# Kernel optimization log

Measured on AMD Instinct MI355X. Metric: run time of the kernel, lower is better.

Reference implementation:

```python
import jax, jax.numpy as jnp
import numpy as np

SEQ_LEN = 128   # sourceL == seq_len
BATCH   = 256
E_DIM   = 512
H_DIM   = 512
C_EXPL  = 10.0  # tanh_exploration


def setup_inputs() -> dict:
    key = jax.random.key(0)
    ks = jax.random.split(key, 24)
    rn = lambda k, shape, s=0.05: (jax.random.normal(k, shape, jnp.float32) * s)
    inp = {
        'decoder_input':  rn(ks[0], (BATCH, E_DIM), 1.0),
        'embedded_inputs': rn(ks[1], (SEQ_LEN, BATCH, E_DIM), 1.0),
        'h0': rn(ks[2], (BATCH, H_DIM), 1.0),
        'c0': rn(ks[3], (BATCH, H_DIM), 1.0),
        'context': rn(ks[4], (SEQ_LEN, BATCH, H_DIM), 1.0),
        # LSTM cell weights (nn.Linear: y = x @ W.T + b)
        'Wi': rn(ks[5], (4 * H_DIM, E_DIM)), 'bi': rn(ks[6], (4 * H_DIM,)),
        'Wh': rn(ks[7], (4 * H_DIM, H_DIM)), 'bh': rn(ks[8], (4 * H_DIM,)),
        # glimpse attention (use_tanh=False)
        'g_Wq': rn(ks[9], (H_DIM, H_DIM)),  'g_bq': rn(ks[10], (H_DIM,)),
        'g_Wref': rn(ks[11], (H_DIM, H_DIM)), 'g_bref': rn(ks[12], (H_DIM,)),
        'g_v': rn(ks[13], (H_DIM,), 1.0 / np.sqrt(H_DIM)),
        # pointer attention (use_tanh=True, C=10)
        'p_Wq': rn(ks[14], (H_DIM, H_DIM)),  'p_bq': rn(ks[15], (H_DIM,)),
        'p_Wref': rn(ks[16], (H_DIM, H_DIM)), 'p_bref': rn(ks[17], (H_DIM,)),
        'p_v': rn(ks[18], (H_DIM,), 1.0 / np.sqrt(H_DIM)),
    }
    return inp


def reference(decoder_input, embedded_inputs, h0, c0, context,
              Wi, bi, Wh, bh,
              g_Wq, g_bq, g_Wref, g_bref, g_v,
              p_Wq, p_bq, p_Wref, p_bref, p_v):
    L, B, H = context.shape

    # Conv1d(k=1) on ref is loop-invariant: precompute e = W_ref @ context, [B,H,L]
    e_g = jnp.einsum('oh,lbh->bol', g_Wref, context) + g_bref[None, :, None]
    e_p = jnp.einsum('oh,lbh->bol', p_Wref, context) + p_bref[None, :, None]
    barange = jnp.arange(B)

    def step(carry, key):
        hx, cx, dec_in, mask, prev = carry
        # fused LSTM cell
        gates = dec_in @ Wi.T + bi + hx @ Wh.T + bh
        i_, f_, g_, o_ = jnp.split(gates, 4, axis=1)
        cy = jax.nn.sigmoid(f_) * cx + jax.nn.sigmoid(i_) * jnp.tanh(g_)
        hy = jax.nn.sigmoid(o_) * jnp.tanh(cy)
        # mark previously selected index as visited
        mask = mask.at[barange, prev].set(True)
        # glimpse (n_glimpses=1, use_tanh=False)
        q = hy @ g_Wq.T + g_bq                                   # [B,H]
        u = jnp.einsum('h,bhl->bl', g_v, jnp.tanh(q[:, :, None] + e_g))
        u = jnp.where(mask, -jnp.inf, u)
        g_l = jnp.einsum('bhl,bl->bh', e_g, jax.nn.softmax(u, axis=1))
        # pointer (use_tanh=True): logits = C * tanh(u), then mask
        q = g_l @ p_Wq.T + p_bq
        u = jnp.einsum('h,bhl->bl', p_v, jnp.tanh(q[:, :, None] + e_p))
        u = jnp.where(mask, -jnp.inf, C_EXPL * jnp.tanh(u))
        probs = jax.nn.softmax(u, axis=1)                        # [B,L]
        # stochastic decode: multinomial sample, gather next embedding
        idxs = jax.random.categorical(key, u, axis=1)            # [B]
        dec_next = embedded_inputs[idxs, barange, :]             # [B,E]
        return (hy, cy, dec_next, mask, idxs), (probs, idxs)

    mask0 = jnp.zeros((B, L), dtype=bool).at[:, 0].set(True)
    prev0 = jnp.zeros((B,), dtype=jnp.int32)
    keys = jax.random.split(jax.random.key(1), L - 1)
    (hy, cy, _, _, _), (probs_seq, idxs_seq) = jax.lax.scan(
        step, (h0, c0, decoder_input, mask0, prev0), keys)

    prob_0 = jnp.zeros((B, L), jnp.float32).at[:, 0].set(1.0)
    outputs = jnp.concatenate([prob_0[None], probs_seq], axis=0)          # [L,B,L]
    selections = jnp.concatenate([prev0[None], idxs_seq], axis=0)         # [L,B]
    return outputs, selections, hy, cy
```

## Files before the change

kernel.cpp:

```cpp
#include <hip/hip_runtime.h>
#include <stdint.h>

#ifndef THREEFRY_PARTITIONABLE
#define THREEFRY_PARTITIONABLE 1
#endif

#define LSEQ 128
#define BSZ  256
#define HD   512
#define G4   2048

#define SEL_OFF  ((size_t)LSEQ * BSZ * LSEQ)
#define HY_OFF   (SEL_OFF + (size_t)LSEQ * BSZ)
#define CY_OFF   (HY_OFF + (size_t)BSZ * HD)

__device__ __forceinline__ uint32_t rotl_(uint32_t v, int r) { return (v << r) | (v >> (32 - r)); }

__device__ __forceinline__ void tf2x32(uint32_t k0, uint32_t k1,
                                       uint32_t x0, uint32_t x1,
                                       uint32_t &o0, uint32_t &o1)
{
  uint32_t k2 = k0 ^ k1 ^ 0x1BD11BDAu;
  x0 += k0; x1 += k1;
#define TFR(r) { x0 += x1; x1 = rotl_(x1,(r)); x1 ^= x0; }
  TFR(13) TFR(15) TFR(26) TFR(6)
  x0 += k1; x1 += k2 + 1u;
  TFR(17) TFR(29) TFR(16) TFR(24)
  x0 += k2; x1 += k0 + 2u;
  TFR(13) TFR(15) TFR(26) TFR(6)
  x0 += k0; x1 += k1 + 3u;
  TFR(17) TFR(29) TFR(16) TFR(24)
  x0 += k1; x1 += k2 + 4u;
  TFR(13) TFR(15) TFR(26) TFR(6)
  x0 += k2; x1 += k0 + 5u;
#undef TFR
  o0 = x0; o1 = x1;
}

__device__ __forceinline__ void step_key(int t, uint32_t &kA, uint32_t &kB)
{
#if THREEFRY_PARTITIONABLE
  uint32_t o0, o1;
  tf2x32(0u, 1u, 0u, (uint32_t)t, o0, o1);
  kA = o0; kB = o1;
#else
  uint32_t o0, o1;
  uint32_t j = 2u * (uint32_t)t;
  if (j < 127u) { tf2x32(0u, 1u, j, 127u + j, o0, o1); kA = o0; }
  else          { tf2x32(0u, 1u, j - 127u, j, o0, o1); kA = o1; }
  j = 2u * (uint32_t)t + 1u;
  if (j < 127u) { tf2x32(0u, 1u, j, 127u + j, o0, o1); kB = o0; }
  else          { tf2x32(0u, 1u, j - 127u, j, o0, o1); kB = o1; }
#endif
}

__device__ __forceinline__ uint32_t draw_bits(uint32_t kA, uint32_t kB, uint32_t n)
{
  uint32_t y0, y1;
#if THREEFRY_PARTITIONABLE
  tf2x32(kA, kB, 0u, n, y0, y1);
  return y0 ^ y1;
#else
  uint32_t i0 = (n < 16384u) ? n : n - 16384u;
  tf2x32(kA, kB, i0, i0 + 16384u, y0, y1);
  return (n < 16384u) ? y0 : y1;
#endif
}

__device__ __forceinline__ float tanh_f(float xf)
{
  float ax = fabsf(xf);
  float z  = fminf(ax * 2.8853900817779268f, 50.0f);
  float e  = __builtin_amdgcn_exp2f(z);
  float d  = e + 1.0f;
  float r0 = __builtin_amdgcn_rcpf(d);
  float r  = fmaf(fmaf(-d, r0, 1.0f), r0, r0);
  return copysignf(fmaf(-2.0f, r, 1.0f), xf);
}

template<int CHUNK>
__global__ __launch_bounds__(512)
void gemm32(const float* __restrict__ A0, const float* __restrict__ A1, int lda,
            const float* __restrict__ B0, const float* __restrict__ B1, int ldb,
            const float* __restrict__ bias,
            double* __restrict__ Cd0, double* __restrict__ Cd1,
            float* __restrict__ Cf0, float* __restrict__ Cf1,
            int N, int K, int out_mode)
{
  constexpr int BM = 64;
  constexpr int BN = 64;
  constexpr int BK = 32;
  __shared__ float As[BK][BM];
  __shared__ float Bs[BK][BN];
  const int tid = threadIdx.x;
  const int tx = tid & 31, ty = tid >> 5;
  const int z = blockIdx.z;
  const float* A = z ? A1 : A0;
  const float* B = z ? B1 : B0;
  const int m0 = blockIdx.x * BM;
  const int n0 = blockIdx.y * BN;

  const int r_ = tid >> 3, kq = (tid & 7) * 4;

  double acc[4][2];
  float  c32[4][2];
#pragma unroll
  for (int i = 0; i < 4; ++i)
#pragma unroll
    for (int j = 0; j < 2; ++j) { acc[i][j] = 0.0; c32[i][j] = 0.0f; }

  const float* bp0 = B + (size_t)(n0 + r_) * ldb + kq;
  float4 w0 = *(const float4*)bp0;
  const float* ap0 = A + (size_t)(m0 + r_) * lda + kq;
  float4 u0 = *(const float4*)ap0;

  for (int k0 = 0; k0 < K; k0 += BK) {
    __syncthreads();
    Bs[kq + 0][r_] = w0.x; Bs[kq + 1][r_] = w0.y;
    Bs[kq + 2][r_] = w0.z; Bs[kq + 3][r_] = w0.w;
    As[kq + 0][r_] = u0.x; As[kq + 1][r_] = u0.y;
    As[kq + 2][r_] = u0.z; As[kq + 3][r_] = u0.w;
    __syncthreads();

    float4 nw0 = w0, nu0 = u0;
    if (k0 + BK < K) {
      nw0 = *(const float4*)(B + (size_t)(n0 + r_) * ldb + (k0 + BK) + kq);
      nu0 = *(const float4*)(A + (size_t)(m0 + r_) * lda + (k0 + BK) + kq);
    }

#pragma unroll
    for (int kk = 0; kk < BK; ++kk) {
      float4 av = *(const float4*)&As[kk][4 * ty];
      float2 bv = *(const float2*)&Bs[kk][2 * tx];
      float a[4] = { av.x, av.y, av.z, av.w };
#pragma unroll
      for (int i = 0; i < 4; ++i) {
        c32[i][0] = fmaf(a[i], bv.x, c32[i][0]);
        c32[i][1] = fmaf(a[i], bv.y, c32[i][1]);
      }
      if ((kk & (CHUNK - 1)) == (CHUNK - 1)) {
#pragma unroll
        for (int i = 0; i < 4; ++i)
#pragma unroll
          for (int j = 0; j < 2; ++j) { acc[i][j] += (double)c32[i][j]; c32[i][j] = 0.0f; }
      }
    }
    w0 = nw0; u0 = nu0;
  }

#pragma unroll
  for (int i = 0; i < 4; ++i) {
    int m = m0 + 4 * ty + i;
#pragma unroll
    for (int j = 0; j < 2; ++j) {
      int n = n0 + 2 * tx + j;
      double v = acc[i][j] + (bias ? (double)bias[n] : 0.0);
      if (out_mode == 0) {
        double* Cd = z ? Cd1 : Cd0;
        Cd[(size_t)m * N + n] = v;
      } else if (out_mode == 1) {
        Cf0[(((size_t)(m & 255)) * LSEQ + (m >> 8)) * HD + n] = (float)v;
      } else if (out_mode == 2) {
        Cf0[(size_t)m * N + n] = (float)v;
      } else if (out_mode == 3) {
        Cf0[(((size_t)(m & 255)) * HD + n) * LSEQ + (m >> 8)] = (float)v;
      } else {
        float* Cf = z ? Cf1 : Cf0;
        Cf[(size_t)m * N + n] = (float)v;
      }
    }
  }
}

__global__ __launch_bounds__(256)
void transpose512(const float* __restrict__ W, float* __restrict__ WT)
{
  __shared__ float tile[32][33];
  int bx = blockIdx.x * 32, by = blockIdx.y * 32;
  int x = threadIdx.x & 31, y = threadIdx.x >> 5;
#pragma unroll
  for (int j = 0; j < 32; j += 8)
    tile[y + j][x] = W[(size_t)(by + y + j) * HD + bx + x];
  __syncthreads();
#pragma unroll
  for (int j = 0; j < 32; j += 8)
    WT[(size_t)(bx + y + j) * HD + by + x] = tile[x][y + j];
}

#define SCOMP(A0_, A1_, A2_, A3_, V4, IT)                         \
  {                                                               \
    const int h_ = (IT) * 16 + hh;                                \
    const float  xq_ = (float)qs[h_];                             \
    const double vv_ = (double)vs[h_];                            \
    A0_ += vv_ * (double)tanh_f(xq_ + (V4).x);                    \
    A1_ += vv_ * (double)tanh_f(xq_ + (V4).y);                    \
    A2_ += vv_ * (double)tanh_f(xq_ + (V4).z);                    \
    A3_ += vv_ * (double)tanh_f(xq_ + (V4).w);                    \
  }

__global__ __launch_bounds__(512)
void step_fused(const float* __restrict__ g0, const float* __restrict__ g1,
                const float* __restrict__ bi, const float* __restrict__ bh,
                const double* __restrict__ c_in, double* __restrict__ c_out,
                float* __restrict__ h_out,
                const float* __restrict__ WqT, const float* __restrict__ g_bq,
                const float* __restrict__ e_g,
                const float* __restrict__ pWqT, const float* __restrict__ p_bq,
                const float* __restrict__ e_p,
                const float* __restrict__ g_v, const float* __restrict__ p_v,
                unsigned char* __restrict__ mask,
                const float* __restrict__ emb, float* __restrict__ dec_in,
                float* __restrict__ out, int t)
{
  const int b   = blockIdx.x;
  const int tid = threadIdx.x;
  const int l   = tid & 127;
  const int lg  = tid & 31;
  const int hh  = tid >> 5;
  __shared__ float  hs[HD];
  __shared__ double qs[HD];
  __shared__ float  vs[HD];
  __shared__ double part[16][LSEQ];
  __shared__ double gls[HD];
  __shared__ double sarr[LSEQ];
  __shared__ double red[4];
  __shared__ double wv[2];
  __shared__ int    wi[2];
  __shared__ int    selidx;

  const float* egbase = e_g + (size_t)b * (HD * LSEQ) + hh * LSEQ + lg * 4;
  const float* epbase = e_p + (size_t)b * (HD * LSEQ) + hh * LSEQ + lg * 4;

  float4 B0[8], B1[8];
#pragma unroll
  for (int j = 0; j < 8; ++j)
    B0[j] = *(const float4*)(egbase + (size_t)j * (16 * LSEQ));

  {
    const int u = tid;
    const size_t base = (size_t)b * G4;
    double gi = (double)g0[base + u]        + (double)g1[base + u]        + (double)bi[u]        + (double)bh[u];
    double gf = (double)g0[base + u + 512]  + (double)g1[base + u + 512]  + (double)bi[u + 512]  + (double)bh[u + 512];
    double gg = (double)g0[base + u + 1024] + (double)g1[base + u + 1024] + (double)bi[u + 1024] + (double)bh[u + 1024];
    double go = (double)g0[base + u + 1536] + (double)g1[base + u + 1536] + (double)bi[u + 1536] + (double)bh[u + 1536];
    double si = 1.0 / (1.0 + exp(-gi));
    double sf = 1.0 / (1.0 + exp(-gf));
    double so = 1.0 / (1.0 + exp(-go));
    double cy = sf * c_in[(size_t)b * HD + u] + si * tanh(gg);
    double hy = so * tanh(cy);
    c_out[(size_t)b * HD + u] = cy;
    float hyf = (float)hy;
    h_out[(size_t)b * HD + u] = hyf;
    hs[u] = hyf;
  }
  __syncthreads();

  {
    const int h = tid;
    const float* wcol = WqT + h;
    float wA[32], wB[32];
    double a = 0.0;
#pragma unroll
    for (int j = 0; j < 32; ++j) wA[j] = wcol[(size_t)j * HD];
#pragma unroll
    for (int pair = 0; pair < 8; ++pair) {
      const int kA = pair * 64;
#pragma unroll
      for (int j = 0; j < 32; ++j) wB[j] = wcol[(size_t)(kA + 32 + j) * HD];
#pragma unroll
      for (int c = 0; c < 4; ++c) {
        float c32 = 0.0f;
#pragma unroll
        for (int j = 0; j < 8; ++j)
          c32 = fmaf(hs[kA + c * 8 + j], wA[c * 8 + j], c32);
        a += (double)c32;
      }
      if (pair < 7) {
#pragma unroll
        for (int j = 0; j < 32; ++j) wA[j] = wcol[(size_t)(kA + 64 + j) * HD];
      }
#pragma unroll
      for (int c = 0; c < 4; ++c) {
        float c32 = 0.0f;
#pragma unroll
        for (int j = 0; j < 8; ++j)
          c32 = fmaf(hs[kA + 32 + c * 8 + j], wB[c * 8 + j], c32);
        a += (double)c32;
      }
    }
    qs[tid] = a + (double)g_bq[tid];
    vs[tid] = g_v[tid];
  }
  __syncthreads();

  {
    double a0 = 0, a1 = 0, a2 = 0, a3 = 0;
#pragma unroll
    for (int j = 0; j < 8; ++j)
      B1[j] = *(const float4*)(egbase + (size_t)(8 + j) * (16 * LSEQ));
#pragma unroll
    for (int j = 0; j < 8; ++j) SCOMP(a0, a1, a2, a3, B0[j], j);
#pragma unroll
    for (int j = 0; j < 8; ++j)
      B0[j] = *(const float4*)(egbase + (size_t)(16 + j) * (16 * LSEQ));
#pragma unroll
    for (int j = 0; j < 8; ++j) SCOMP(a0, a1, a2, a3, B1[j], 8 + j);
#pragma unroll
    for (int j = 0; j < 8; ++j)
      B1[j] = *(const float4*)(egbase + (size_t)(24 + j) * (16 * LSEQ));
#pragma unroll
    for (int j = 0; j < 8; ++j) SCOMP(a0, a1, a2, a3, B0[j], 16 + j);
#pragma unroll
    for (int j = 0; j < 8; ++j) SCOMP(a0, a1, a2, a3, B1[j], 24 + j);
    part[hh][lg * 4 + 0] = a0;
    part[hh][lg * 4 + 1] = a1;
    part[hh][lg * 4 + 2] = a2;
    part[hh][lg * 4 + 3] = a3;
  }
  __syncthreads();

  bool   msk = false;
  double u = 0.0, pe = 0.0;
  if (tid < 128) {
    msk = mask[(size_t)b * LSEQ + l] != 0;
    u = 0.0;
#pragma unroll
    for (int o = 0; o < 16; ++o) u += part[o][l];
    if (msk) u = -__builtin_inf();
    double mx = u;
    for (int off = 32; off; off >>= 1) mx = fmax(mx, __shfl_xor(mx, off));
    if ((tid & 63) == 0) red[tid >> 6] = mx;
  }
  __syncthreads();
  if (tid < 128) {
    double mx = fmax(red[0], red[1]);
    pe = msk ? 0.0 : exp(u - mx);
    double sm = pe;
    for (int off = 32; off; off >>= 1) sm += __shfl_xor(sm, off);
    if ((tid & 63) == 0) red[2 + (tid >> 6)] = sm;
  }
  __syncthreads();
  if (tid < 128) sarr[l] = pe / (red[2] + red[3]);
  __syncthreads();

  {
#pragma unroll
    for (int j = 0; j < 8; ++j)
      B0[j] = *(const float4*)(epbase + (size_t)j * (16 * LSEQ));

    const float4* row = (const float4*)(e_g + ((size_t)b * HD + tid) * LSEQ);
    float4 rA[4], rB[4];
    double a = 0.0;
#pragma unroll
    for (int j = 0; j < 4; ++j) rA[j] = row[j];
#pragma unroll
    for (int r = 0; r < 4; ++r) {
#pragma unroll
      for (int j = 0; j < 4; ++j) rB[j] = row[r * 8 + 4 + j];
#pragma unroll
      for (int j = 0; j < 4; ++j) {
        int l4 = (r * 8 + j) * 4;
        float4 v = rA[j];
        a += (double)v.x * sarr[l4 + 0];
        a += (double)v.y * sarr[l4 + 1];
        a += (double)v.z * sarr[l4 + 2];
        a += (double)v.w * sarr[l4 + 3];
      }
      if (r < 3) {
#pragma unroll
        for (int j = 0; j < 4; ++j) rA[j] = row[r * 8 + 8 + j];
      }
#pragma unroll
      for (int j = 0; j < 4; ++j) {
        int l4 = (r * 8 + 4 + j) * 4;
        float4 v = rB[j];
        a += (double)v.x * sarr[l4 + 0];
        a += (double)v.y * sarr[l4 + 1];
        a += (double)v.z * sarr[l4 + 2];
        a += (double)v.w * sarr[l4 + 3];
      }
    }
    gls[tid] = a;
  }
  __syncthreads();

  {
    const float* wcol = pWqT + tid;
    float wA[32], wB[32];
    double a = 0.0;
#pragma unroll
    for (int j = 0; j < 32; ++j) wA[j] = wcol[(size_t)j * HD];
#pragma unroll
    for (int pair = 0; pair < 8; ++pair) {
      const int hA = pair * 64;
#pragma unroll
      for (int j = 0; j < 32; ++j) wB[j] = wcol[(size_t)(hA + 32 + j) * HD];
#pragma unroll
      for (int j = 0; j < 32; ++j) a += gls[hA + j] * (double)wA[j];
      if (pair < 7) {
#pragma unroll
        for (int j = 0; j < 32; ++j) wA[j] = wcol[(size_t)(hA + 64 + j) * HD];
      }
#pragma unroll
      for (int j = 0; j < 32; ++j) a += gls[hA + 32 + j] * (double)wB[j];
    }
    qs[tid] = a + (double)p_bq[tid];
    vs[tid] = p_v[tid];
  }
  __syncthreads();

  {
    double a0 = 0, a1 = 0, a2 = 0, a3 = 0;
#pragma unroll
    for (int j = 0; j < 8; ++j)
      B1[j] = *(const float4*)(epbase + (size_t)(8 + j) * (16 * LSEQ));
#pragma unroll
    for (int j = 0; j < 8; ++j) SCOMP(a0, a1, a2, a3, B0[j], j);
#pragma unroll
    for (int j = 0; j < 8; ++j)
      B0[j] = *(const float4*)(epbase + (size_t)(16 + j) * (16 * LSEQ));
#pragma unroll
    for (int j = 0; j < 8; ++j) SCOMP(a0, a1, a2, a3, B1[j], 8 + j);
#pragma unroll
    for (int j = 0; j < 8; ++j)
      B1[j] = *(const float4*)(epbase + (size_t)(24 + j) * (16 * LSEQ));
#pragma unroll
    for (int j = 0; j < 8; ++j) SCOMP(a0, a1, a2, a3, B0[j], 16 + j);
#pragma unroll
    for (int j = 0; j < 8; ++j) SCOMP(a0, a1, a2, a3, B1[j], 24 + j);
    part[hh][lg * 4 + 0] = a0;
    part[hh][lg * 4 + 1] = a1;
    part[hh][lg * 4 + 2] = a2;
    part[hh][lg * 4 + 3] = a3;
  }
  __syncthreads();

  double logit = 0.0, cand = 0.0;
  int idx = l;
  if (tid < 128) {
    double acc2 = 0.0;
#pragma unroll
    for (int o = 0; o < 16; ++o) acc2 += part[o][l];
    logit = msk ? -__builtin_inf() : 10.0 * tanh(acc2);
    double mx = logit;
    for (int off = 32; off; off >>= 1) mx = fmax(mx, __shfl_xor(mx, off));
    if ((tid & 63) == 0) red[tid >> 6] = mx;
  }
  __syncthreads();
  if (tid < 128) {
    double mx = fmax(red[0], red[1]);
    double pe2 = msk ? 0.0 : exp(logit - mx);
    double sm = pe2;
    for (int off = 32; off; off >>= 1) sm += __shfl_xor(sm, off);
    if ((tid & 63) == 0) red[2 + (tid >> 6)] = sm;
  }
  __syncthreads();
  if (tid < 128) {
    double mx = fmax(red[0], red[1]);
    double pe2 = msk ? 0.0 : exp(logit - mx);
    out[(size_t)(t + 1) * BSZ * LSEQ + (size_t)b * LSEQ + l] = (float)(pe2 / (red[2] + red[3]));

    uint32_t kA, kB;
    step_key(t, kA, kB);
    uint32_t bits = draw_bits(kA, kB, (uint32_t)(b * LSEQ + l));
    float f = __uint_as_float((bits >> 9) | 0x3f800000u) - 1.0f;
    const float TINY = 1.17549435e-38f;
    float uu = fmaxf(f * (1.0f - TINY) + TINY, TINY);
    float gmb = -logf(-logf(uu));
    cand = msk ? -__builtin_inf() : (logit + (double)gmb);

    for (int off = 32; off; off >>= 1) {
      double c2 = __shfl_xor(cand, off);
      int    i2 = __shfl_xor(idx, off);
      if (c2 > cand || (c2 == cand && i2 < idx)) { cand = c2; idx = i2; }
    }
    if ((tid & 63) == 0) { wv[tid >> 6] = cand; wi[tid >> 6] = idx; }
  }
  __syncthreads();
  if (tid == 0) {
    double c2 = wv[1]; int i2 = wi[1];
    if (c2 > cand || (c2 == cand && i2 < idx)) { cand = c2; idx = i2; }
    selidx = idx;
    out[SEL_OFF + (size_t)(t + 1) * BSZ + b] = (float)idx;
    mask[(size_t)b * LSEQ + idx] = 1;
  }
  __syncthreads();
  {
    int sidx = selidx;
    dec_in[(size_t)b * HD + tid] = emb[((size_t)sidx * BSZ + b) * HD + tid];
  }
}

__global__ __launch_bounds__(256)
void init_kernel(const float* __restrict__ dec0, const float* __restrict__ h0,
                 const float* __restrict__ c0, float* __restrict__ dec_in,
                 float* __restrict__ hf, double* __restrict__ c,
                 unsigned char* __restrict__ mask, float* __restrict__ out)
{
  int i = blockIdx.x * blockDim.x + threadIdx.x;
  if (i < BSZ * HD) { hf[i] = h0[i]; c[i] = (double)c0[i]; dec_in[i] = dec0[i]; }
  if (i < BSZ * LSEQ) {
    mask[i] = ((i & (LSEQ - 1)) == 0) ? 1 : 0;
    out[i] = ((i & (LSEQ - 1)) == 0) ? 1.0f : 0.0f;
  }
  if (i < BSZ) out[SEL_OFF + i] = 0.0f;
}

__global__ __launch_bounds__(256)
void finalize(const float* __restrict__ hf, const double* __restrict__ c,
              float* __restrict__ out)
{
  int i = blockIdx.x * blockDim.x + threadIdx.x;
  if (i < BSZ * HD) {
    out[HY_OFF + i] = hf[i];
    out[CY_OFF + i] = (float)c[i];
  }
}

extern "C" void kernel_launch(void* const* d_in, const int* in_sizes, int n_in,
                              void* d_out, int out_size, void* d_ws, size_t ws_size,
                              hipStream_t stream)
{
  (void)in_sizes; (void)n_in; (void)out_size; (void)ws_size;
  const float* dec0  = (const float*)d_in[0];
  const float* emb   = (const float*)d_in[1];
  const float* h0    = (const float*)d_in[2];
  const float* c0    = (const float*)d_in[3];
  const float* ctx   = (const float*)d_in[4];
  const float* Wi    = (const float*)d_in[5];
  const float* bi    = (const float*)d_in[6];
  const float* Wh    = (const float*)d_in[7];
  const float* bh    = (const float*)d_in[8];
  const float* gWq   = (const float*)d_in[9];
  const float* gbq   = (const float*)d_in[10];
  const float* gWref = (const float*)d_in[11];
  const float* gbref = (const float*)d_in[12];
  const float* gv    = (const float*)d_in[13];
  const float* pWq   = (const float*)d_in[14];
  const float* pbq   = (const float*)d_in[15];
  const float* pWref = (const float*)d_in[16];
  const float* pbref = (const float*)d_in[17];
  const float* pv    = (const float*)d_in[18];
  float* out = (float*)d_out;

  char* ws = (char*)d_ws;
  size_t off = 0;
  auto take = [&](size_t bytes) -> char* {
    char* p = ws + off;
    off += (bytes + 255) & ~(size_t)255;
    return p;
  };
  float*  e_g   = (float*) take((size_t)BSZ * LSEQ * HD * 4);
  float*  e_p   = (float*) take((size_t)BSZ * LSEQ * HD * 4);
  float*  g0f   = (float*) take((size_t)BSZ * G4 * 4);
  float*  g1f   = (float*) take((size_t)BSZ * G4 * 4);
  double* cb0   = (double*)take((size_t)BSZ * HD * 8);
  double* cb1   = (double*)take((size_t)BSZ * HD * 8);
  float*  hf0   = (float*) take((size_t)BSZ * HD * 4);
  float*  hf1   = (float*) take((size_t)BSZ * HD * 4);
  float*  WqT   = (float*) take((size_t)HD * HD * 4);
  float*  pWqT  = (float*) take((size_t)HD * HD * 4);
  float*  decb  = (float*) take((size_t)BSZ * HD * 4);
  unsigned char* mask = (unsigned char*)take((size_t)BSZ * LSEQ);

  init_kernel<<<512, 256, 0, stream>>>(dec0, h0, c0, decb, hf0, cb0, mask, out);
  transpose512<<<dim3(16, 16), 256, 0, stream>>>(gWq, WqT);
  transpose512<<<dim3(16, 16), 256, 0, stream>>>(pWq, pWqT);

  gemm32<8><<<dim3(BSZ * LSEQ / 64, HD / 64, 1), 512, 0, stream>>>(
      ctx, nullptr, HD, gWref, nullptr, HD, gbref,
      nullptr, nullptr, e_g, nullptr, HD, HD, 3);
  gemm32<8><<<dim3(BSZ * LSEQ / 64, HD / 64, 1), 512, 0, stream>>>(
      ctx, nullptr, HD, pWref, nullptr, HD, pbref,
      nullptr, nullptr, e_p, nullptr, HD, HD, 3);

  double* cb[2] = { cb0, cb1 };
  float*  hf[2] = { hf0, hf1 };
  for (int t = 0; t < LSEQ - 1; ++t) {
    int rs = t & 1, wsl = rs ^ 1;
    gemm32<8><<<dim3(BSZ / 64, G4 / 64, 2), 512, 0, stream>>>(
        decb, hf[rs], HD, Wi, Wh, HD, nullptr,
        nullptr, nullptr, g0f, g1f, G4, HD, 4);
    step_fused<<<BSZ, 512, 0, stream>>>(g0f, g1f, bi, bh,
                                        cb[rs], cb[wsl], hf[wsl],
                                        WqT, gbq, e_g, pWqT, pbq, e_p, gv, pv,
                                        mask, emb, decb, out, t);
  }
  finalize<<<BSZ * HD / 256, 256, 0, stream>>>(hf[1], cb[1], out);
}
```

Before: 13.03 ms.

## Double-buffer GEMM shared tiles and collapse softmax reductions into one wavefront

The GEMM kernel now keeps two shared-memory tiles, so the next K-slice is stored into the alternate buffer after compute and only one barrier per iteration is needed. In the per-step fused kernel, the glimpse and pointer softmax/argmax reductions now run in a single 64-lane wavefront with two elements per lane. This drops the cross-wave shared-memory reduction arrays and several __syncthreads. The pointer e_p prefetch is hoisted earlier and the glimpse row loads are widened to 8 float4s. The trade-off is more registers and double the GEMM LDS, and a single wave now does twice the serial exp/tanh/RNG work.

```diff
diff --git a/kernel.cpp b/kernel.cpp
--- a/kernel.cpp
+++ b/kernel.cpp
@@ -90,8 +90,8 @@
   constexpr int BM = 64;
   constexpr int BN = 64;
   constexpr int BK = 32;
-  __shared__ float As[BK][BM];
-  __shared__ float Bs[BK][BN];
+  __shared__ float As[2][BK][BM];
+  __shared__ float Bs[2][BK][BN];
   const int tid = threadIdx.x;
   const int tx = tid & 31, ty = tid >> 5;
   const int z = blockIdx.z;
@@ -109,29 +109,30 @@
 #pragma unroll
     for (int j = 0; j < 2; ++j) { acc[i][j] = 0.0; c32[i][j] = 0.0f; }
 
-  const float* bp0 = B + (size_t)(n0 + r_) * ldb + kq;
-  float4 w0 = *(const float4*)bp0;
-  const float* ap0 = A + (size_t)(m0 + r_) * lda + kq;
-  float4 u0 = *(const float4*)ap0;
-
-  for (int k0 = 0; k0 < K; k0 += BK) {
-    __syncthreads();
-    Bs[kq + 0][r_] = w0.x; Bs[kq + 1][r_] = w0.y;
-    Bs[kq + 2][r_] = w0.z; Bs[kq + 3][r_] = w0.w;
-    As[kq + 0][r_] = u0.x; As[kq + 1][r_] = u0.y;
-    As[kq + 2][r_] = u0.z; As[kq + 3][r_] = u0.w;
-    __syncthreads();
-
-    float4 nw0 = w0, nu0 = u0;
-    if (k0 + BK < K) {
-      nw0 = *(const float4*)(B + (size_t)(n0 + r_) * ldb + (k0 + BK) + kq);
-      nu0 = *(const float4*)(A + (size_t)(m0 + r_) * lda + (k0 + BK) + kq);
+  {
+    float4 w0 = *(const float4*)(B + (size_t)(n0 + r_) * ldb + kq);
+    float4 u0 = *(const float4*)(A + (size_t)(m0 + r_) * lda + kq);
+    Bs[0][kq + 0][r_] = w0.x; Bs[0][kq + 1][r_] = w0.y;
+    Bs[0][kq + 2][r_] = w0.z; Bs[0][kq + 3][r_] = w0.w;
+    As[0][kq + 0][r_] = u0.x; As[0][kq + 1][r_] = u0.y;
+    As[0][kq + 2][r_] = u0.z; As[0][kq + 3][r_] = u0.w;
+  }
+  __syncthreads();
+
+  const int NT = K / BK;
+  for (int t = 0; t < NT; ++t) {
+    const int cur = t & 1;
+    float4 nw, nu;
+    const bool more = (t + 1 < NT);
+    if (more) {
+      nw = *(const float4*)(B + (size_t)(n0 + r_) * ldb + (t + 1) * BK + kq);
+      nu = *(const float4*)(A + (size_t)(m0 + r_) * lda + (t + 1) * BK + kq);
     }
 
 #pragma unroll
     for (int kk = 0; kk < BK; ++kk) {
-      float4 av = *(const float4*)&As[kk][4 * ty];
-      float2 bv = *(const float2*)&Bs[kk][2 * tx];
+      float4 av = *(const float4*)&As[cur][kk][4 * ty];
+      float2 bv = *(const float2*)&Bs[cur][kk][2 * tx];
       float a[4] = { av.x, av.y, av.z, av.w };
 #pragma unroll
       for (int i = 0; i < 4; ++i) {
@@ -145,7 +146,15 @@
           for (int j = 0; j < 2; ++j) { acc[i][j] += (double)c32[i][j]; c32[i][j] = 0.0f; }
       }
     }
-    w0 = nw0; u0 = nu0;
+
+    if (more) {
+      const int nxt = cur ^ 1;
+      Bs[nxt][kq + 0][r_] = nw.x; Bs[nxt][kq + 1][r_] = nw.y;
+      Bs[nxt][kq + 2][r_] = nw.z; Bs[nxt][kq + 3][r_] = nw.w;
+      As[nxt][kq + 0][r_] = nu.x; As[nxt][kq + 1][r_] = nu.y;
+      As[nxt][kq + 2][r_] = nu.z; As[nxt][kq + 3][r_] = nu.w;
+    }
+    __syncthreads();
   }
 
 #pragma unroll
@@ -214,7 +223,6 @@
 {
   const int b   = blockIdx.x;
   const int tid = threadIdx.x;
-  const int l   = tid & 127;
   const int lg  = tid & 31;
   const int hh  = tid >> 5;
   __shared__ float  hs[HD];
@@ -223,9 +231,6 @@
   __shared__ double part[16][LSEQ];
   __shared__ double gls[HD];
   __shared__ double sarr[LSEQ];
-  __shared__ double red[4];
-  __shared__ double wv[2];
-  __shared__ int    wi[2];
   __shared__ int    selidx;
 
   const float* egbase = e_g + (size_t)b * (HD * LSEQ) + hh * LSEQ + lg * 4;
@@ -317,62 +322,58 @@
     part[hh][lg * 4 + 2] = a2;
     part[hh][lg * 4 + 3] = a3;
   }
-  __syncthreads();
-
-  bool   msk = false;
-  double u = 0.0, pe = 0.0;
-  if (tid < 128) {
-    msk = mask[(size_t)b * LSEQ + l] != 0;
-    u = 0.0;
-#pragma unroll
-    for (int o = 0; o < 16; ++o) u += part[o][l];
-    if (msk) u = -__builtin_inf();
-    double mx = u;
+
+#pragma unroll
+  for (int j = 0; j < 8; ++j)
+    B0[j] = *(const float4*)(epbase + (size_t)j * (16 * LSEQ));
+  __syncthreads();
+
+  bool msk0 = false, msk1 = false;
+  if (tid < 64) {
+    msk0 = mask[(size_t)b * LSEQ + tid] != 0;
+    msk1 = mask[(size_t)b * LSEQ + tid + 64] != 0;
+    double u0 = 0.0, u1 = 0.0;
+#pragma unroll
+    for (int o = 0; o < 16; ++o) { u0 += part[o][tid]; u1 += part[o][tid + 64]; }
+    if (msk0) u0 = -__builtin_inf();
+    if (msk1) u1 = -__builtin_inf();
+    double mx = fmax(u0, u1);
     for (int off = 32; off; off >>= 1) mx = fmax(mx, __shfl_xor(mx, off));
-    if ((tid & 63) == 0) red[tid >> 6] = mx;
-  }
-  __syncthreads();
-  if (tid < 128) {
-    double mx = fmax(red[0], red[1]);
-    pe = msk ? 0.0 : exp(u - mx);
-    double sm = pe;
+    double pe0 = msk0 ? 0.0 : exp(u0 - mx);
+    double pe1 = msk1 ? 0.0 : exp(u1 - mx);
+    double sm = pe0 + pe1;
     for (int off = 32; off; off >>= 1) sm += __shfl_xor(sm, off);
-    if ((tid & 63) == 0) red[2 + (tid >> 6)] = sm;
-  }
-  __syncthreads();
-  if (tid < 128) sarr[l] = pe / (red[2] + red[3]);
-  __syncthreads();
-
-  {
-#pragma unroll
-    for (int j = 0; j < 8; ++j)
-      B0[j] = *(const float4*)(epbase + (size_t)j * (16 * LSEQ));
-
+    sarr[tid]      = pe0 / sm;
+    sarr[tid + 64] = pe1 / sm;
+  }
+  __syncthreads();
+
+  {
     const float4* row = (const float4*)(e_g + ((size_t)b * HD + tid) * LSEQ);
-    float4 rA[4], rB[4];
+    float4 rA[8], rB[8];
     double a = 0.0;
 #pragma unroll
-    for (int j = 0; j < 4; ++j) rA[j] = row[j];
-#pragma unroll
-    for (int r = 0; r < 4; ++r) {
-#pragma unroll
-      for (int j = 0; j < 4; ++j) rB[j] = row[r * 8 + 4 + j];
-#pragma unroll
-      for (int j = 0; j < 4; ++j) {
-        int l4 = (r * 8 + j) * 4;
+    for (int j = 0; j < 8; ++j) rA[j] = row[j];
+#pragma unroll
+    for (int r = 0; r < 2; ++r) {
+#pragma unroll
+      for (int j = 0; j < 8; ++j) rB[j] = row[r * 16 + 8 + j];
+#pragma unroll
+      for (int j = 0; j < 8; ++j) {
+        int l4 = (r * 16 + j) * 4;
         float4 v = rA[j];
         a += (double)v.x * sarr[l4 + 0];
         a += (double)v.y * sarr[l4 + 1];
         a += (double)v.z * sarr[l4 + 2];
         a += (double)v.w * sarr[l4 + 3];
       }
-      if (r < 3) {
-#pragma unroll
-        for (int j = 0; j < 4; ++j) rA[j] = row[r * 8 + 8 + j];
-      }
-#pragma unroll
-      for (int j = 0; j < 4; ++j) {
-        int l4 = (r * 8 + 4 + j) * 4;
+      if (r < 1) {
+#pragma unroll
+        for (int j = 0; j < 8; ++j) rA[j] = row[r * 16 + 16 + j];
+      }
+#pragma unroll
+      for (int j = 0; j < 8; ++j) {
+        int l4 = (r * 16 + 8 + j) * 4;
         float4 v = rB[j];
         a += (double)v.x * sarr[l4 + 0];
         a += (double)v.y * sarr[l4 + 1];
@@ -435,54 +436,50 @@
   }
   __syncthreads();
 
-  double logit = 0.0, cand = 0.0;
-  int idx = l;
-  if (tid < 128) {
-    double acc2 = 0.0;
-#pragma unroll
-    for (int o = 0; o < 16; ++o) acc2 += part[o][l];
-    logit = msk ? -__builtin_inf() : 10.0 * tanh(acc2);
-    double mx = logit;
+  if (tid < 64) {
+    double a20 = 0.0, a21 = 0.0;
+#pragma unroll
+    for (int o = 0; o < 16; ++o) { a20 += part[o][tid]; a21 += part[o][tid + 64]; }
+    double lt0 = msk0 ? -__builtin_inf() : 10.0 * tanh(a20);
+    double lt1 = msk1 ? -__builtin_inf() : 10.0 * tanh(a21);
+    double mx = fmax(lt0, lt1);
     for (int off = 32; off; off >>= 1) mx = fmax(mx, __shfl_xor(mx, off));
-    if ((tid & 63) == 0) red[tid >> 6] = mx;
-  }
-  __syncthreads();
-  if (tid < 128) {
-    double mx = fmax(red[0], red[1]);
-    double pe2 = msk ? 0.0 : exp(logit - mx);
-    double sm = pe2;
+    double pq0 = msk0 ? 0.0 : exp(lt0 - mx);
+    double pq1 = msk1 ? 0.0 : exp(lt1 - mx);
+    double sm = pq0 + pq1;
     for (int off = 32; off; off >>= 1) sm += __shfl_xor(sm, off);
-    if ((tid & 63) == 0) red[2 + (tid >> 6)] = sm;
-  }
-  __syncthreads();
-  if (tid < 128) {
-    double mx = fmax(red[0], red[1]);
-    double pe2 = msk ? 0.0 : exp(logit - mx);
-    out[(size_t)(t + 1) * BSZ * LSEQ + (size_t)b * LSEQ + l] = (float)(pe2 / (red[2] + red[3]));
+    size_t obase = (size_t)(t + 1) * BSZ * LSEQ + (size_t)b * LSEQ;
+    out[obase + tid]      = (float)(pq0 / sm);
+    out[obase + tid + 64] = (float)(pq1 / sm);
 
     uint32_t kA, kB;
     step_key(t, kA, kB);
-    uint32_t bits = draw_bits(kA, kB, (uint32_t)(b * LSEQ + l));
-    float f = __uint_as_float((bits >> 9) | 0x3f800000u) - 1.0f;
     const float TINY = 1.17549435e-38f;
-    float uu = fmaxf(f * (1.0f - TINY) + TINY, TINY);
-    float gmb = -logf(-logf(uu));
-    cand = msk ? -__builtin_inf() : (logit + (double)gmb);
-
+    uint32_t bits0 = draw_bits(kA, kB, (uint32_t)(b * LSEQ + tid));
+    uint32_t bits1 = draw_bits(kA, kB, (uint32_t)(b * LSEQ + tid + 64));
+    float f0 = __uint_as_float((bits0 >> 9) | 0x3f800000u) - 1.0f;
+    float f1 = __uint_as_float((bits1 >> 9) | 0x3f800000u) - 1.0f;
+    float uu0 = fmaxf(f0 * (1.0f - TINY) + TINY, TINY);
+    float uu1 = fmaxf(f1 * (1.0f - TINY) + TINY, TINY);
+    float gm0 = -logf(-logf(uu0));
+    float gm1 = -logf(-logf(uu1));
+    double cand0 = msk0 ? -__builtin_inf() : (lt0 + (double)gm0);
+    double cand1 = msk1 ? -__builtin_inf() : (lt1 + (double)gm1);
+
+    double cand;
+    int idx;
+    if (cand1 > cand0) { cand = cand1; idx = tid + 64; }
+    else               { cand = cand0; idx = tid; }
     for (int off = 32; off; off >>= 1) {
       double c2 = __shfl_xor(cand, off);
       int    i2 = __shfl_xor(idx, off);
       if (c2 > cand || (c2 == cand && i2 < idx)) { cand = c2; idx = i2; }
     }
-    if ((tid & 63) == 0) { wv[tid >> 6] = cand; wi[tid >> 6] = idx; }
-  }
-  __syncthreads();
-  if (tid == 0) {
-    double c2 = wv[1]; int i2 = wi[1];
-    if (c2 > cand || (c2 == cand && i2 < idx)) { cand = c2; idx = i2; }
-    selidx = idx;
-    out[SEL_OFF + (size_t)(t + 1) * BSZ + b] = (float)idx;
-    mask[(size_t)b * LSEQ + idx] = 1;
+    if (tid == 0) {
+      selidx = idx;
+      out[SEL_OFF + (size_t)(t + 1) * BSZ + b] = (float)idx;
+      mask[(size_t)b * LSEQ + idx] = 1;
+    }
   }
   __syncthreads();
   {
```

Measured after the change: 13.86 ms. 6.3% more time.
